# Performance work log

Hardware: AMD Instinct MI355X
Metric: run time of the kernel (lower is better)

The kernel has to match this reference:

```python
import jax, jax.numpy as jnp
import numpy as np

N_LAYERS = 12
N_HEADS = 12
D_MODEL = 768
VOCAB = 50257
T_WIN = 1024
B, T = 4, 1024
STD = 0.02


def setup_inputs() -> dict:
    key = jax.random.key(0)
    ks = jax.random.split(key, 8)
    inp = jax.random.randint(ks[0], (B, T), 0, VOCAB)
    target = jax.random.randint(ks[1], (B, T), 0, VOCAB)
    wte = jax.random.normal(ks[2], (VOCAB, D_MODEL), jnp.float32) * STD
    wpe = jax.random.normal(ks[3], (T_WIN, D_MODEL), jnp.float32) * STD
    attn_w = jax.random.normal(ks[4], (N_LAYERS, D_MODEL, 3 * D_MODEL), jnp.float32) * STD
    proj_w = jax.random.normal(ks[5], (N_LAYERS, D_MODEL, D_MODEL), jnp.float32) * STD
    fc_w = jax.random.normal(ks[6], (N_LAYERS, D_MODEL, 4 * D_MODEL), jnp.float32) * STD
    fc2_w = jax.random.normal(ks[7], (N_LAYERS, 4 * D_MODEL, D_MODEL), jnp.float32) * STD
    return {
        'inp': inp, 'target': target, 'wte': wte, 'wpe': wpe,
        'ln1_w': jnp.ones((N_LAYERS, D_MODEL), jnp.float32),
        'ln1_b': jnp.zeros((N_LAYERS, D_MODEL), jnp.float32),
        'attn_w': attn_w,
        'attn_b': jnp.zeros((N_LAYERS, 3 * D_MODEL), jnp.float32),
        'proj_w': proj_w,
        'proj_b': jnp.zeros((N_LAYERS, D_MODEL), jnp.float32),
        'ln2_w': jnp.ones((N_LAYERS, D_MODEL), jnp.float32),
        'ln2_b': jnp.zeros((N_LAYERS, D_MODEL), jnp.float32),
        'fc_w': fc_w,
        'fc_b': jnp.zeros((N_LAYERS, 4 * D_MODEL), jnp.float32),
        'fc2_w': fc2_w,
        'fc2_b': jnp.zeros((N_LAYERS, D_MODEL), jnp.float32),
        'lnf_w': jnp.ones((D_MODEL,), jnp.float32),
        'lnf_b': jnp.zeros((D_MODEL,), jnp.float32),
    }


def _layernorm(x, w, b, eps=1e-5):
    mu = jnp.mean(x, axis=-1, keepdims=True)
    var = jnp.var(x, axis=-1, keepdims=True)
    return (x - mu) * jax.lax.rsqrt(var + eps) * w + b


def _attention(x, w_qkv, b_qkv, w_proj, b_proj):
    b, t, c = x.shape
    hd = c // N_HEADS
    qkv = x @ w_qkv + b_qkv                      # [B,T,3C]
    q, k, v = jnp.split(qkv, 3, axis=-1)
    # [B,H,T,hd]
    q = q.reshape(b, t, N_HEADS, hd).transpose(0, 2, 1, 3)
    k = k.reshape(b, t, N_HEADS, hd).transpose(0, 2, 1, 3)
    v = v.reshape(b, t, N_HEADS, hd).transpose(0, 2, 1, 3)
    scores = jnp.einsum('bhqd,bhkd->bhqk', q, k) / jnp.sqrt(jnp.float32(hd))
    causal = jnp.tril(jnp.ones((t, t), bool))
    scores = jnp.where(causal[None, None], scores, -jnp.inf)
    w = jax.nn.softmax(scores, axis=-1)          # dropout p=0 (eval)
    ctx = jnp.einsum('bhqk,bhkd->bhqd', w, v)
    ctx = ctx.transpose(0, 2, 1, 3).reshape(b, t, c)
    return ctx @ w_proj + b_proj


def reference(inp, target, wte, wpe, ln1_w, ln1_b, attn_w, attn_b, proj_w, proj_b,
              ln2_w, ln2_b, fc_w, fc_b, fc2_w, fc2_b, lnf_w, lnf_b):
    b, t = inp.shape
    x = wte[inp] + wpe[:t][None]                 # [B,T,C]
    for i in range(N_LAYERS):
        x = x + _attention(_layernorm(x, ln1_w[i], ln1_b[i]),
                           attn_w[i], attn_b[i], proj_w[i], proj_b[i])
        h = _layernorm(x, ln2_w[i], ln2_b[i])
        h = jax.nn.gelu(h @ fc_w[i] + fc_b[i], approximate=True)
        x = x + (h @ fc2_w[i] + fc2_b[i])
    x = _layernorm(x, lnf_w, lnf_b)
    logits = x @ wte.T                            # tied lm_head, no bias
    logp = jax.nn.log_softmax(logits, axis=-1)
    nll = -jnp.take_along_axis(logp, target[..., None], axis=-1)[..., 0]
    loss = jnp.mean(nll)
    return logits, loss
```

## Files before the change

kernel.cpp:

```cpp
#include <hip/hip_runtime.h>
#include <hip/hip_bf16.h>
#include <cmath>

#define NLAYERS 12
#define NHEADS  12
#define DM      768
#define VOCAB   50257
#define TSEQ    1024
#define BT      4096
#define NCHUNK  786

typedef __attribute__((ext_vector_type(4))) float f32x4;
typedef __attribute__((ext_vector_type(8))) short bf16x8;

typedef __hip_bfloat16 bf16;

#define MFMA16(a, b, c) __builtin_amdgcn_mfma_f32_16x16x32_bf16(a, b, c, 0, 0, 0)

__device__ __forceinline__ void gload16(const void* g, void* l) {
    __builtin_amdgcn_global_load_lds(
        (const __attribute__((address_space(1))) void*)g,
        (__attribute__((address_space(3))) void*)l, 16, 0, 0);
}

__device__ __forceinline__ void wg_barrier() {
    asm volatile("" ::: "memory");
    __builtin_amdgcn_s_barrier();
    asm volatile("" ::: "memory");
}

__device__ __forceinline__ float gelu_tanh(float v) {
    float u = 0.7978845608028654f * (v + 0.044715f * v * v * v);
    return 0.5f * v * (1.0f + tanhf(u));
}

__device__ __forceinline__ short f2bf(float f) {
    bf16 h = (bf16)f;
    return *reinterpret_cast<short*>(&h);
}

struct ushort4s { short a, b, c, d; };

__global__ void transpose_bf16_kernel(const float* __restrict__ in, bf16* __restrict__ out,
                                      int K, int N) {
    __shared__ float tile[32][33];
    size_t lofs = (size_t)blockIdx.z * K * N;
    int k0 = blockIdx.y * 32, n0 = blockIdx.x * 32;
    int tx = threadIdx.x, ty = threadIdx.y;
#pragma unroll
    for (int i = 0; i < 32; i += 8)
        tile[ty + i][tx] = in[lofs + (size_t)(k0 + ty + i) * N + n0 + tx];
    __syncthreads();
#pragma unroll
    for (int i = 0; i < 32; i += 8)
        out[lofs + (size_t)(n0 + ty + i) * K + k0 + tx] = (bf16)tile[tx][ty + i];
}

__global__ void tobf16_kernel(const float* __restrict__ in, bf16* __restrict__ out, size_t n) {
    size_t i = (size_t)blockIdx.x * 256 + threadIdx.x;
    if (i < n) out[i] = (bf16)in[i];
}

__global__ void embed_kernel(const int* __restrict__ inp, const float* __restrict__ wte,
                             const float* __restrict__ wpe, float* __restrict__ x) {
    int idx = blockIdx.x * 256 + threadIdx.x;
    int m = idx / (DM / 4), c4 = idx % (DM / 4);
    int tok = inp[m];
    int t = m & (TSEQ - 1);
    float4 a = reinterpret_cast<const float4*>(wte)[(size_t)tok * (DM / 4) + c4];
    float4 b = reinterpret_cast<const float4*>(wpe)[(size_t)t * (DM / 4) + c4];
    float4 o = {a.x + b.x, a.y + b.y, a.z + b.z, a.w + b.w};
    reinterpret_cast<float4*>(x)[idx] = o;
}

__global__ __launch_bounds__(256) void ln_kernel(const float* __restrict__ x,
                                                 const float* __restrict__ w,
                                                 const float* __restrict__ b,
                                                 bf16* __restrict__ y) {
    int row = blockIdx.x, tid = threadIdx.x;
    const float4* xr = reinterpret_cast<const float4*>(x + (size_t)row * DM);
    float4 v = {0.f, 0.f, 0.f, 0.f};
    float s = 0.f, q = 0.f;
    if (tid < 192) {
        v = xr[tid];
        s = v.x + v.y + v.z + v.w;
        q = v.x * v.x + v.y * v.y + v.z * v.z + v.w * v.w;
    }
#pragma unroll
    for (int o = 1; o < 64; o <<= 1) { s += __shfl_xor(s, o); q += __shfl_xor(q, o); }
    __shared__ float ss[4], qq[4];
    if ((tid & 63) == 0) { ss[tid >> 6] = s; qq[tid >> 6] = q; }
    __syncthreads();
    s = ss[0] + ss[1] + ss[2] + ss[3];
    q = qq[0] + qq[1] + qq[2] + qq[3];
    float mu  = s * (1.0f / DM);
    float var = q * (1.0f / DM) - mu * mu;
    float inv = rsqrtf(var + 1e-5f);
    if (tid < 192) {
        float4 wv = reinterpret_cast<const float4*>(w)[tid];
        float4 bv = reinterpret_cast<const float4*>(b)[tid];
        ushort4s o;
        o.a = f2bf((v.x - mu) * inv * wv.x + bv.x);
        o.b = f2bf((v.y - mu) * inv * wv.y + bv.y);
        o.c = f2bf((v.z - mu) * inv * wv.z + bv.z);
        o.d = f2bf((v.w - mu) * inv * wv.w + bv.w);
        *reinterpret_cast<ushort4s*>(y + (size_t)row * DM + tid * 4) = o;
    }
}

#define GF_GELU    1
#define GF_OBF16   2
#define GF_CLAMP   4
#define GF_PARTIAL 8

template<int FLAGS, int TAG>
__global__ __launch_bounds__(256) void gemm_k(
    const bf16* __restrict__ A, const bf16* __restrict__ Bt,
    const float* __restrict__ bias, const float* __restrict__ resid,
    void* __restrict__ C, float2* __restrict__ partials,
    int M, int N, int K) {
    __shared__ short ldsA[2][128 * 32];
    __shared__ short ldsB[2][128 * 32];
    int tid = threadIdx.x;
    int lane = tid & 63, w = tid >> 6;
    int wm = w >> 1, wn = w & 1;
    int r = lane & 15, kq = lane >> 4;
    int bm = blockIdx.x * 128, bn = blockIdx.y * 128;

    f32x4 acc[4][4] = {};

    auto stage = [&](int buf, int k0) {
#pragma unroll
        for (int i = 0; i < 2; ++i) {
            int chunk = i * 256 + tid;
            int row = chunk >> 2;
            int gs = (chunk & 3) ^ ((row >> 1) & 3);
            const bf16* ga = A + (size_t)(bm + row) * K + k0 + gs * 8;
            gload16(ga, &ldsA[buf][(i * 256 + w * 64) * 8]);
            int brow = bn + row;
            if (FLAGS & GF_CLAMP) brow = min(brow, N - 1);
            const bf16* gb = Bt + (size_t)brow * K + k0 + gs * 8;
            gload16(gb, &ldsB[buf][(i * 256 + w * 64) * 8]);
        }
    };
    auto compute = [&](int buf) {
        bf16x8 af[4], bfr[4];
#pragma unroll
        for (int m = 0; m < 4; ++m) {
            int row = wm * 64 + m * 16 + r;
            af[m] = *reinterpret_cast<bf16x8*>(&ldsA[buf][row * 32 + (kq ^ ((row >> 1) & 3)) * 8]);
        }
#pragma unroll
        for (int n = 0; n < 4; ++n) {
            int row = wn * 64 + n * 16 + r;
            bfr[n] = *reinterpret_cast<bf16x8*>(&ldsB[buf][row * 32 + (kq ^ ((row >> 1) & 3)) * 8]);
        }
#pragma unroll
        for (int m = 0; m < 4; ++m)
#pragma unroll
            for (int n = 0; n < 4; ++n)
                acc[m][n] = MFMA16(af[m], bfr[n], acc[m][n]);
    };

    stage(0, 0);
    __syncthreads();
    int buf = 0;
    for (int k0 = 32; k0 < K; k0 += 32) {
        stage(buf ^ 1, k0);
        compute(buf);
        __syncthreads();
        buf ^= 1;
    }
    compute(buf);

    int row0 = bm + wm * 64, col0 = bn + wn * 64;
#pragma unroll
    for (int m = 0; m < 4; ++m) {
#pragma unroll
        for (int n = 0; n < 4; ++n) {
            int col = col0 + n * 16 + r;
            if (col < N) {
#pragma unroll
                for (int rr = 0; rr < 4; ++rr) {
                    int row = row0 + m * 16 + kq * 4 + rr;
                    float v = acc[m][n][rr];
                    if (bias) v += bias[col];
                    if (FLAGS & GF_GELU) v = gelu_tanh(v);
                    if (resid) v += resid[(size_t)row * N + col];
                    if (FLAGS & GF_OBF16) ((bf16*)C)[(size_t)row * N + col] = (bf16)v;
                    else                  ((float*)C)[(size_t)row * N + col] = v;
                }
            }
        }
    }
}

template<int FLAGS, int TAG>
__global__ __launch_bounds__(512, 1) void gemm256_8p(
    const bf16* __restrict__ A, const bf16* __restrict__ Bt,
    const float* __restrict__ bias, const float* __restrict__ resid,
    void* __restrict__ C, float2* __restrict__ partials,
    int M, int N, int K) {
    __shared__ short lds[2][2][256 * 64];
    int tid = threadIdx.x;
    int lane = tid & 63, w = tid >> 6;
    int wm = w >> 2, wn = w & 3;
    int r = lane & 15, kq = lane >> 4;
    int bm = blockIdx.x * 256, bn = blockIdx.y * 256;

    f32x4 acc[8][4] = {};

    auto stage_half = [&](int buf, int kt, int half) {
        int mat = half >> 1;
        int hrow = (half & 1) * 128;
        const bf16* src = mat ? Bt : A;
        int base = mat ? bn : bm;
#pragma unroll
        for (int i = 0; i < 2; ++i) {
            int chunk = i * 512 + tid;
            int lrow = hrow + (chunk >> 3);
            int gsrc = (chunk & 7) ^ (lrow & 7);
            int grow = base + lrow;
            if (mat && (FLAGS & GF_CLAMP)) grow = min(grow, N - 1);
            gload16(src + (size_t)grow * K + kt * 64 + gsrc * 8,
                    &lds[buf][mat][hrow * 64 + chunk * 8]);
        }
    };

    auto do_phase = [&](int buf, int p) {
        int mh = p >> 1, nh = p & 1;
        bf16x8 bfr[2][2], af[4][2];
#pragma unroll
        for (int n2 = 0; n2 < 2; ++n2) {
            int row = wn * 64 + (nh * 2 + n2) * 16 + r;
#pragma unroll
            for (int kk = 0; kk < 2; ++kk) {
                int lg = kk * 4 + kq;
                bfr[n2][kk] = *reinterpret_cast<bf16x8*>(
                    &lds[buf][1][row * 64 + (lg ^ (row & 7)) * 8]);
            }
        }
#pragma unroll
        for (int m2 = 0; m2 < 4; ++m2) {
            int row = wm * 128 + (mh * 4 + m2) * 16 + r;
#pragma unroll
            for (int kk = 0; kk < 2; ++kk) {
                int lg = kk * 4 + kq;
                af[m2][kk] = *reinterpret_cast<bf16x8*>(
                    &lds[buf][0][row * 64 + (lg ^ (row & 7)) * 8]);
            }
        }
        __builtin_amdgcn_s_setprio(1);
#pragma unroll
        for (int m2 = 0; m2 < 4; ++m2)
#pragma unroll
            for (int n2 = 0; n2 < 2; ++n2)
#pragma unroll
                for (int kk = 0; kk < 2; ++kk)
                    acc[mh * 4 + m2][nh * 2 + n2] =
                        MFMA16(af[m2][kk], bfr[n2][kk], acc[mh * 4 + m2][nh * 2 + n2]);
        __builtin_amdgcn_s_setprio(0);
    };

    const int NT = K / 64;
    stage_half(0, 0, 0); stage_half(0, 0, 1); stage_half(0, 0, 2); stage_half(0, 0, 3);
    for (int t = 0; t < NT; ++t) {
        int buf = t & 1;
        bool more = (t + 1 < NT);
        if (more) { stage_half(buf ^ 1, t + 1, 0); stage_half(buf ^ 1, t + 1, 1); }
        if (more) asm volatile("s_waitcnt vmcnt(4)" ::: "memory");
        else      asm volatile("s_waitcnt vmcnt(0)" ::: "memory");
        wg_barrier();
        do_phase(buf, 0);
        wg_barrier();
        if (more) { stage_half(buf ^ 1, t + 1, 2); stage_half(buf ^ 1, t + 1, 3); }
        do_phase(buf, 1);
        wg_barrier();
        do_phase(buf, 2);
        wg_barrier();
        do_phase(buf, 3);
        wg_barrier();
    }

    int row0 = bm + wm * 128, col0 = bn + wn * 64;
#pragma unroll
    for (int m = 0; m < 8; ++m) {
#pragma unroll
        for (int n = 0; n < 4; ++n) {
            int col = col0 + n * 16 + r;
            if (col < N) {
#pragma unroll
                for (int rr = 0; rr < 4; ++rr) {
                    int row = row0 + m * 16 + kq * 4 + rr;
                    float v = acc[m][n][rr];
                    if (bias) v += bias[col];
                    if (FLAGS & GF_GELU) v = gelu_tanh(v);
                    if (resid) v += resid[(size_t)row * N + col];
                    if (FLAGS & GF_OBF16) ((bf16*)C)[(size_t)row * N + col] = (bf16)v;
                    else                  ((float*)C)[(size_t)row * N + col] = v;
                }
            }
        }
    }

    if (FLAGS & GF_PARTIAL) {
        int chunk = (bn >> 6) + wn;
        if (chunk < NCHUNK) {
#pragma unroll
            for (int m = 0; m < 8; ++m) {
#pragma unroll
                for (int rr = 0; rr < 4; ++rr) {
                    float vals[4], mx = -INFINITY;
#pragma unroll
                    for (int n = 0; n < 4; ++n) {
                        int col = col0 + n * 16 + r;
                        float v = (col < N) ? acc[m][n][rr] : -INFINITY;
                        vals[n] = v;
                        mx = fmaxf(mx, v);
                    }
#pragma unroll
                    for (int o = 1; o < 16; o <<= 1) mx = fmaxf(mx, __shfl_xor(mx, o));
                    float sum = 0.f;
#pragma unroll
                    for (int n = 0; n < 4; ++n)
                        if (vals[n] > -INFINITY) sum += __expf(vals[n] - mx);
#pragma unroll
                    for (int o = 1; o < 16; o <<= 1) sum += __shfl_xor(sum, o);
                    if (r == 0) {
                        int row = row0 + m * 16 + kq * 4 + rr;
                        partials[(size_t)row * NCHUNK + chunk] = make_float2(mx, sum);
                    }
                }
            }
        }
    }
}

__global__ __launch_bounds__(256) void flash_attn_kernel(const bf16* __restrict__ qkv,
                                                         bf16* __restrict__ ctx) {
    __shared__ short Ks[128 * 64];
    __shared__ short Vt[64][132];
    __shared__ short Ps[4][16][132];

    int tid = threadIdx.x, lane = tid & 63, w = tid >> 6;
    int r = lane & 15, kq = lane >> 4;
    int q0 = blockIdx.x * 64;
    int bh = blockIdx.y;
    int b = bh / NHEADS, h = bh % NHEADS;
    const int RS = 3 * DM;

    const bf16* qbase = qkv + (size_t)(b * TSEQ + q0 + w * 16 + r) * RS + h * 64;
    bf16x8 qf[2];
    qf[0] = *reinterpret_cast<const bf16x8*>(qbase + kq * 8);
    qf[1] = *reinterpret_cast<const bf16x8*>(qbase + 32 + kq * 8);

    f32x4 of[4] = {};
    float mrow[4] = {-INFINITY, -INFINITY, -INFINITY, -INFINITY};
    float lrow[4] = {};

    int ntiles = (blockIdx.x >> 1) + 1;
    for (int t = 0; t < ntiles; ++t) {
        int kv0 = t * 128;
        __syncthreads();
        const bf16* kbase = qkv + (size_t)(b * TSEQ + kv0) * RS + DM + h * 64;
#pragma unroll
        for (int i = 0; i < 4; ++i) {
            int chunk = i * 256 + tid;
            int row = chunk >> 3, cp = chunk & 7;
            int csrc = cp ^ (row & 7);
            gload16(kbase + (size_t)row * RS + csrc * 8, Ks + chunk * 8);
        }
        const bf16* vbase = qkv + (size_t)(b * TSEQ + kv0) * RS + 2 * DM + h * 64;
#pragma unroll
        for (int i = 0; i < 4; ++i) {
            int chunk = i * 256 + tid;
            int kv = chunk >> 3, d0 = (chunk & 7) * 8;
            bf16x8 v = *reinterpret_cast<const bf16x8*>(vbase + (size_t)kv * RS + d0);
#pragma unroll
            for (int j = 0; j < 8; ++j) Vt[d0 + j][kv] = ((short*)&v)[j];
        }
        __syncthreads();

        f32x4 sf[8];
#pragma unroll
        for (int n = 0; n < 8; ++n) sf[n] = (f32x4){0.f, 0.f, 0.f, 0.f};
        __builtin_amdgcn_s_setprio(1);
#pragma unroll
        for (int n = 0; n < 8; ++n) {
            int row = n * 16 + r;
#pragma unroll
            for (int kt = 0; kt < 2; ++kt) {
                int gran = (kt * 4 + kq) ^ (row & 7);
                bf16x8 kf = *reinterpret_cast<bf16x8*>(&Ks[row * 64 + gran * 8]);
                sf[n] = MFMA16(qf[kt], kf, sf[n]);
            }
        }
        __builtin_amdgcn_s_setprio(0);

        bool diag = (kv0 + 128 > q0);
        float alpha[4];
#pragma unroll
        for (int rr = 0; rr < 4; ++rr) {
            int qrow = q0 + w * 16 + kq * 4 + rr;
            float vals[8];
            float mx = mrow[rr];
#pragma unroll
            for (int n = 0; n < 8; ++n) {
                float v = sf[n][rr] * 0.125f;
                if (diag && (kv0 + n * 16 + r) > qrow) v = -INFINITY;
                vals[n] = v;
                mx = fmaxf(mx, v);
            }
#pragma unroll
            for (int o = 1; o < 16; o <<= 1) mx = fmaxf(mx, __shfl_xor(mx, o));
            float al = __expf(mrow[rr] - mx);
            float sum = 0.f;
#pragma unroll
            for (int n = 0; n < 8; ++n) {
                float p = __expf(vals[n] - mx);
                vals[n] = p;
                sum += p;
            }
#pragma unroll
            for (int o = 1; o < 16; o <<= 1) sum += __shfl_xor(sum, o);
            mrow[rr] = mx;
            lrow[rr] = lrow[rr] * al + sum;
            alpha[rr] = al;
#pragma unroll
            for (int n = 0; n < 8; ++n) Ps[w][kq * 4 + rr][n * 16 + r] = f2bf(vals[n]);
        }
#pragma unroll
        for (int n = 0; n < 4; ++n)
#pragma unroll
            for (int rr = 0; rr < 4; ++rr) of[n][rr] *= alpha[rr];

        __builtin_amdgcn_s_setprio(1);
#pragma unroll
        for (int kt = 0; kt < 4; ++kt) {
            bf16x8 pa = *reinterpret_cast<bf16x8*>(&Ps[w][r][kt * 32 + kq * 8]);
#pragma unroll
            for (int n = 0; n < 4; ++n) {
                bf16x8 vf = *reinterpret_cast<bf16x8*>(&Vt[n * 16 + r][kt * 32 + kq * 8]);
                of[n] = MFMA16(pa, vf, of[n]);
            }
        }
        __builtin_amdgcn_s_setprio(0);
    }

#pragma unroll
    for (int rr = 0; rr < 4; ++rr) {
        float inv = 1.0f / lrow[rr];
        int qrow = q0 + w * 16 + kq * 4 + rr;
        bf16* cb = ctx + (size_t)(b * TSEQ + qrow) * DM + h * 64;
#pragma unroll
        for (int n = 0; n < 4; ++n) cb[n * 16 + r] = (bf16)(of[n][rr] * inv);
    }
}

__global__ __launch_bounds__(256) void loss_reduce_kernel(const float2* __restrict__ partials,
                                                          const float* __restrict__ logits,
                                                          const int* __restrict__ target,
                                                          float* __restrict__ nll) {
    int row = blockIdx.x, tid = threadIdx.x;
    const float2* pr = partials + (size_t)row * NCHUNK;
    float m = -INFINITY, s = 0.f;
    for (int c = tid; c < NCHUNK; c += 256) {
        float2 p = pr[c];
        if (p.x > m) { s = s * __expf(m - p.x) + p.y; m = p.x; }
        else         { s += p.y * __expf(p.x - m); }
    }
    __shared__ float sm[256], ssum[256];
    sm[tid] = m; ssum[tid] = s; __syncthreads();
    for (int o = 128; o; o >>= 1) {
        if (tid < o) {
            float m2 = sm[tid + o], s2 = ssum[tid + o];
            float mm = fmaxf(sm[tid], m2);
            ssum[tid] = ssum[tid] * __expf(sm[tid] - mm) + s2 * __expf(m2 - mm);
            sm[tid] = mm;
        }
        __syncthreads();
    }
    if (tid == 0) {
        float lse = sm[0] + logf(ssum[0]);
        nll[row] = lse - logits[(size_t)row * VOCAB + target[row]];
    }
}

__global__ void loss2_kernel(const float* __restrict__ nll, float* __restrict__ loss) {
    int tid = threadIdx.x;
    float s = 0.f;
    for (int i = tid; i < BT; i += 1024) s += nll[i];
    __shared__ float r[1024];
    r[tid] = s; __syncthreads();
    for (int o = 512; o; o >>= 1) { if (tid < o) r[tid] += r[tid + o]; __syncthreads(); }
    if (tid == 0) *loss = r[0] * (1.0f / BT);
}

extern "C" void kernel_launch(void* const* d_in, const int* in_sizes, int n_in,
                              void* d_out, int out_size, void* d_ws, size_t ws_size,
                              hipStream_t stream) {
    const int*   inp    = (const int*)  d_in[0];
    const int*   target = (const int*)  d_in[1];
    const float* wte    = (const float*)d_in[2];
    const float* wpe    = (const float*)d_in[3];
    const float* ln1_w  = (const float*)d_in[4];
    const float* ln1_b  = (const float*)d_in[5];
    const float* attn_w = (const float*)d_in[6];
    const float* attn_b = (const float*)d_in[7];
    const float* proj_w = (const float*)d_in[8];
    const float* proj_b = (const float*)d_in[9];
    const float* ln2_w  = (const float*)d_in[10];
    const float* ln2_b  = (const float*)d_in[11];
    const float* fc_w   = (const float*)d_in[12];
    const float* fc_b   = (const float*)d_in[13];
    const float* fc2_w  = (const float*)d_in[14];
    const float* fc2_b  = (const float*)d_in[15];
    const float* lnf_w  = (const float*)d_in[16];
    const float* lnf_b  = (const float*)d_in[17];
    float* out = (float*)d_out;

    char* p = (char*)d_ws;
    auto alloc = [&](size_t bytes) { char* q = p; p += (bytes + 255) & ~(size_t)255; return q; };
    float* x     = (float*)alloc((size_t)BT * DM * 4);
    float* nll   = (float*)alloc((size_t)BT * 4);
    bf16*  qkvb  = (bf16*) alloc((size_t)BT * 3 * DM * 2);
    bf16*  tmpb  = (bf16*) alloc((size_t)BT * DM * 2);
    bf16*  ctxb  = (bf16*) alloc((size_t)BT * DM * 2);
    bf16*  hb    = (bf16*) alloc((size_t)BT * 4 * DM * 2);
    bf16*  wteb  = (bf16*) alloc((size_t)VOCAB * DM * 2);
    bf16*  wqkvT = (bf16*) alloc((size_t)NLAYERS * 3 * DM * DM * 2);
    bf16*  wprojT= (bf16*) alloc((size_t)NLAYERS * DM * DM * 2);
    bf16*  wfcT  = (bf16*) alloc((size_t)NLAYERS * 4 * DM * DM * 2);
    bf16*  wfc2T = (bf16*) alloc((size_t)NLAYERS * 4 * DM * DM * 2);
    float2* partials = (float2*)ctxb;

    dim3 tb(32, 8);
    transpose_bf16_kernel<<<dim3(3 * DM / 32, DM / 32, NLAYERS), tb, 0, stream>>>(attn_w, wqkvT, DM, 3 * DM);
    transpose_bf16_kernel<<<dim3(DM / 32, DM / 32, NLAYERS), tb, 0, stream>>>(proj_w, wprojT, DM, DM);
    transpose_bf16_kernel<<<dim3(4 * DM / 32, DM / 32, NLAYERS), tb, 0, stream>>>(fc_w, wfcT, DM, 4 * DM);
    transpose_bf16_kernel<<<dim3(DM / 32, 4 * DM / 32, NLAYERS), tb, 0, stream>>>(fc2_w, wfc2T, 4 * DM, DM);
    {
        size_t n = (size_t)VOCAB * DM;
        tobf16_kernel<<<(unsigned)((n + 255) / 256), 256, 0, stream>>>(wte, wteb, n);
    }

    embed_kernel<<<BT * DM / 4 / 256, 256, 0, stream>>>(inp, wte, wpe, x);

    for (int i = 0; i < NLAYERS; ++i) {
        ln_kernel<<<BT, 256, 0, stream>>>(x, ln1_w + i * DM, ln1_b + i * DM, tmpb);
        gemm_k<GF_OBF16, 0><<<dim3(BT / 128, 3 * DM / 128), 256, 0, stream>>>(
            tmpb, wqkvT + (size_t)i * 3 * DM * DM, attn_b + i * 3 * DM, nullptr,
            qkvb, nullptr, BT, 3 * DM, DM);
        flash_attn_kernel<<<dim3(TSEQ / 64, 4 * NHEADS), 256, 0, stream>>>(qkvb, ctxb);
        gemm_k<0, 1><<<dim3(BT / 128, DM / 128), 256, 0, stream>>>(
            ctxb, wprojT + (size_t)i * DM * DM, proj_b + i * DM, x,
            x, nullptr, BT, DM, DM);
        ln_kernel<<<BT, 256, 0, stream>>>(x, ln2_w + i * DM, ln2_b + i * DM, tmpb);
        gemm_k<GF_GELU | GF_OBF16, 2><<<dim3(BT / 128, 4 * DM / 128), 256, 0, stream>>>(
            tmpb, wfcT + (size_t)i * 4 * DM * DM, fc_b + i * 4 * DM, nullptr,
            hb, nullptr, BT, 4 * DM, DM);
        gemm_k<0, 3><<<dim3(BT / 128, DM / 128), 256, 0, stream>>>(
            hb, wfc2T + (size_t)i * 4 * DM * DM, fc2_b + i * DM, x,
            x, nullptr, BT, DM, 4 * DM);
    }

    ln_kernel<<<BT, 256, 0, stream>>>(x, lnf_w, lnf_b, tmpb);
    gemm256_8p<GF_CLAMP | GF_PARTIAL, 4><<<dim3(BT / 256, (VOCAB + 255) / 256), 512, 0, stream>>>(
        tmpb, wteb, nullptr, nullptr, out, partials, BT, VOCAB, DM);
    loss_reduce_kernel<<<BT, 256, 0, stream>>>(partials, out, target, nll);
    loss2_kernel<<<1, 1024, 0, stream>>>(nll, out + (size_t)out_size - 1);
}
```

Baseline: 4.290 ms.

## Software-pipeline GEMM fragment loads and swizzle V transpose in flash attention

The 256x256 GEMM now loads the LDS fragments for the next phase while the current phase's MFMAs run, and prefetches the next tile's first fragments at the end of each iteration. The global-load wait moves later in the loop, and launch bounds are raised to allow two blocks per CU. Flash attention now builds the transposed V tile with 4-element packed stores into an XOR-swizzled layout instead of scalar stores into a padded array, to cut LDS bank conflicts and store count. The cost is higher register pressure from holding two fragment sets, which may conflict with the 2-block occupancy target and cause spills.

```diff
diff --git a/kernel.cpp b/kernel.cpp
--- a/kernel.cpp
+++ b/kernel.cpp
@@ -12,6 +12,7 @@
 
 typedef __attribute__((ext_vector_type(4))) float f32x4;
 typedef __attribute__((ext_vector_type(8))) short bf16x8;
+typedef __attribute__((ext_vector_type(4))) short s16x4;
 
 typedef __hip_bfloat16 bf16;
 
@@ -196,7 +197,7 @@
 }
 
 template<int FLAGS, int TAG>
-__global__ __launch_bounds__(512, 1) void gemm256_8p(
+__global__ __launch_bounds__(512, 2) void gemm256_8p(
     const bf16* __restrict__ A, const bf16* __restrict__ Bt,
     const float* __restrict__ bias, const float* __restrict__ resid,
     void* __restrict__ C, float2* __restrict__ partials,
@@ -227,29 +228,30 @@
         }
     };
 
-    auto do_phase = [&](int buf, int p) {
+    struct Frags { bf16x8 a[4][2]; bf16x8 b[2][2]; };
+
+    auto ld_frags = [&](int buf, int p, Frags& F) {
         int mh = p >> 1, nh = p & 1;
-        bf16x8 bfr[2][2], af[4][2];
 #pragma unroll
         for (int n2 = 0; n2 < 2; ++n2) {
             int row = wn * 64 + (nh * 2 + n2) * 16 + r;
 #pragma unroll
-            for (int kk = 0; kk < 2; ++kk) {
-                int lg = kk * 4 + kq;
-                bfr[n2][kk] = *reinterpret_cast<bf16x8*>(
-                    &lds[buf][1][row * 64 + (lg ^ (row & 7)) * 8]);
-            }
+            for (int kk = 0; kk < 2; ++kk)
+                F.b[n2][kk] = *reinterpret_cast<bf16x8*>(
+                    &lds[buf][1][row * 64 + ((kk * 4 + kq) ^ (row & 7)) * 8]);
         }
 #pragma unroll
         for (int m2 = 0; m2 < 4; ++m2) {
             int row = wm * 128 + (mh * 4 + m2) * 16 + r;
 #pragma unroll
-            for (int kk = 0; kk < 2; ++kk) {
-                int lg = kk * 4 + kq;
-                af[m2][kk] = *reinterpret_cast<bf16x8*>(
-                    &lds[buf][0][row * 64 + (lg ^ (row & 7)) * 8]);
-            }
-        }
+            for (int kk = 0; kk < 2; ++kk)
+                F.a[m2][kk] = *reinterpret_cast<bf16x8*>(
+                    &lds[buf][0][row * 64 + ((kk * 4 + kq) ^ (row & 7)) * 8]);
+        }
+    };
+
+    auto do_mfma = [&](int p, Frags& F) {
+        int mh = p >> 1, nh = p & 1;
         __builtin_amdgcn_s_setprio(1);
 #pragma unroll
         for (int m2 = 0; m2 < 4; ++m2)
@@ -258,27 +260,34 @@
 #pragma unroll
                 for (int kk = 0; kk < 2; ++kk)
                     acc[mh * 4 + m2][nh * 2 + n2] =
-                        MFMA16(af[m2][kk], bfr[n2][kk], acc[mh * 4 + m2][nh * 2 + n2]);
+                        MFMA16(F.a[m2][kk], F.b[n2][kk], acc[mh * 4 + m2][nh * 2 + n2]);
         __builtin_amdgcn_s_setprio(0);
     };
 
     const int NT = K / 64;
     stage_half(0, 0, 0); stage_half(0, 0, 1); stage_half(0, 0, 2); stage_half(0, 0, 3);
+    asm volatile("s_waitcnt vmcnt(0)" ::: "memory");
+    wg_barrier();
+    Frags cur, nxt;
+    ld_frags(0, 0, cur);
+
     for (int t = 0; t < NT; ++t) {
         int buf = t & 1;
         bool more = (t + 1 < NT);
+        do_mfma(0, cur);
         if (more) { stage_half(buf ^ 1, t + 1, 0); stage_half(buf ^ 1, t + 1, 1); }
-        if (more) asm volatile("s_waitcnt vmcnt(4)" ::: "memory");
-        else      asm volatile("s_waitcnt vmcnt(0)" ::: "memory");
+        ld_frags(buf, 1, nxt);
         wg_barrier();
-        do_phase(buf, 0);
+        do_mfma(1, nxt);
+        if (more) { stage_half(buf ^ 1, t + 1, 2); stage_half(buf ^ 1, t + 1, 3); }
+        ld_frags(buf, 2, cur);
         wg_barrier();
-        if (more) { stage_half(buf ^ 1, t + 1, 2); stage_half(buf ^ 1, t + 1, 3); }
-        do_phase(buf, 1);
+        do_mfma(2, cur);
+        if (more) asm volatile("s_waitcnt vmcnt(0)" ::: "memory");
+        ld_frags(buf, 3, nxt);
         wg_barrier();
-        do_phase(buf, 2);
-        wg_barrier();
-        do_phase(buf, 3);
+        do_mfma(3, nxt);
+        if (more) ld_frags(buf ^ 1, 0, cur);
         wg_barrier();
     }
 
@@ -339,7 +348,7 @@
 __global__ __launch_bounds__(256) void flash_attn_kernel(const bf16* __restrict__ qkv,
                                                          bf16* __restrict__ ctx) {
     __shared__ short Ks[128 * 64];
-    __shared__ short Vt[64][132];
+    __shared__ short Vt[64 * 128];
     __shared__ short Ps[4][16][132];
 
     int tid = threadIdx.x, lane = tid & 63, w = tid >> 6;
@@ -371,13 +380,21 @@
             gload16(kbase + (size_t)row * RS + csrc * 8, Ks + chunk * 8);
         }
         const bf16* vbase = qkv + (size_t)(b * TSEQ + kv0) * RS + 2 * DM + h * 64;
-#pragma unroll
-        for (int i = 0; i < 4; ++i) {
-            int chunk = i * 256 + tid;
-            int kv = chunk >> 3, d0 = (chunk & 7) * 8;
-            bf16x8 v = *reinterpret_cast<const bf16x8*>(vbase + (size_t)kv * RS + d0);
-#pragma unroll
-            for (int j = 0; j < 8; ++j) Vt[d0 + j][kv] = ((short*)&v)[j];
+        {
+            int kvq = tid >> 3;
+            int d0 = (tid & 7) * 8;
+            bf16x8 v0 = *reinterpret_cast<const bf16x8*>(vbase + (size_t)(kvq * 4 + 0) * RS + d0);
+            bf16x8 v1 = *reinterpret_cast<const bf16x8*>(vbase + (size_t)(kvq * 4 + 1) * RS + d0);
+            bf16x8 v2 = *reinterpret_cast<const bf16x8*>(vbase + (size_t)(kvq * 4 + 2) * RS + d0);
+            bf16x8 v3 = *reinterpret_cast<const bf16x8*>(vbase + (size_t)(kvq * 4 + 3) * RS + d0);
+            int lg = kvq >> 1, half = kvq & 1;
+#pragma unroll
+            for (int j = 0; j < 8; ++j) {
+                int d = d0 + j;
+                int phys = lg ^ (d & 7);
+                s16x4 pk = {v0[j], v1[j], v2[j], v3[j]};
+                *reinterpret_cast<s16x4*>(&Vt[d * 128 + phys * 8 + half * 4]) = pk;
+            }
         }
         __syncthreads();
 
@@ -440,7 +457,9 @@
             bf16x8 pa = *reinterpret_cast<bf16x8*>(&Ps[w][r][kt * 32 + kq * 8]);
 #pragma unroll
             for (int n = 0; n < 4; ++n) {
-                bf16x8 vf = *reinterpret_cast<bf16x8*>(&Vt[n * 16 + r][kt * 32 + kq * 8]);
+                int row = n * 16 + r;
+                int gran = (kt * 4 + kq) ^ (row & 7);
+                bf16x8 vf = *reinterpret_cast<bf16x8*>(&Vt[row * 128 + gran * 8]);
                 of[n] = MFMA16(pa, vf, of[n]);
             }
         }
```

After: 4.341 ms. About the same (+1.2%).

## Prefetch K/V via registers in flash attention and use one-wave-per-row layernorm

Applied to the files above, without the earlier changes.

Flash attention now loads the next K/V tile into registers while the current tile computes, then writes K and a transposed V into LDS using a swizzled layout without padding. The goal is to hide global load latency and cut bank conflicts on the V transpose. LayerNorm now processes four rows per block, one wavefront per row, which removes the LDS reduction and the block barrier. The register prefetch raises VGPR pressure in the attention kernel and could lower occupancy.

```diff
diff --git a/kernel.cpp b/kernel.cpp
--- a/kernel.cpp
+++ b/kernel.cpp
@@ -12,6 +12,7 @@
 
 typedef __attribute__((ext_vector_type(4))) float f32x4;
 typedef __attribute__((ext_vector_type(8))) short bf16x8;
+typedef __attribute__((ext_vector_type(4))) short s16x4;
 
 typedef __hip_bfloat16 bf16;
 
@@ -77,34 +78,33 @@
                                                  const float* __restrict__ w,
                                                  const float* __restrict__ b,
                                                  bf16* __restrict__ y) {
-    int row = blockIdx.x, tid = threadIdx.x;
+    int tid = threadIdx.x, wv = tid >> 6, lane = tid & 63;
+    int row = blockIdx.x * 4 + wv;
     const float4* xr = reinterpret_cast<const float4*>(x + (size_t)row * DM);
-    float4 v = {0.f, 0.f, 0.f, 0.f};
+    float4 v[3];
     float s = 0.f, q = 0.f;
-    if (tid < 192) {
-        v = xr[tid];
-        s = v.x + v.y + v.z + v.w;
-        q = v.x * v.x + v.y * v.y + v.z * v.z + v.w * v.w;
+#pragma unroll
+    for (int j = 0; j < 3; ++j) {
+        v[j] = xr[lane + 64 * j];
+        s += v[j].x + v[j].y + v[j].z + v[j].w;
+        q += v[j].x * v[j].x + v[j].y * v[j].y + v[j].z * v[j].z + v[j].w * v[j].w;
     }
 #pragma unroll
     for (int o = 1; o < 64; o <<= 1) { s += __shfl_xor(s, o); q += __shfl_xor(q, o); }
-    __shared__ float ss[4], qq[4];
-    if ((tid & 63) == 0) { ss[tid >> 6] = s; qq[tid >> 6] = q; }
-    __syncthreads();
-    s = ss[0] + ss[1] + ss[2] + ss[3];
-    q = qq[0] + qq[1] + qq[2] + qq[3];
     float mu  = s * (1.0f / DM);
     float var = q * (1.0f / DM) - mu * mu;
     float inv = rsqrtf(var + 1e-5f);
-    if (tid < 192) {
-        float4 wv = reinterpret_cast<const float4*>(w)[tid];
-        float4 bv = reinterpret_cast<const float4*>(b)[tid];
+#pragma unroll
+    for (int j = 0; j < 3; ++j) {
+        int c4 = lane + 64 * j;
+        float4 wv4 = reinterpret_cast<const float4*>(w)[c4];
+        float4 bv4 = reinterpret_cast<const float4*>(b)[c4];
         ushort4s o;
-        o.a = f2bf((v.x - mu) * inv * wv.x + bv.x);
-        o.b = f2bf((v.y - mu) * inv * wv.y + bv.y);
-        o.c = f2bf((v.z - mu) * inv * wv.z + bv.z);
-        o.d = f2bf((v.w - mu) * inv * wv.w + bv.w);
-        *reinterpret_cast<ushort4s*>(y + (size_t)row * DM + tid * 4) = o;
+        o.a = f2bf((v[j].x - mu) * inv * wv4.x + bv4.x);
+        o.b = f2bf((v[j].y - mu) * inv * wv4.y + bv4.y);
+        o.c = f2bf((v[j].z - mu) * inv * wv4.z + bv4.z);
+        o.d = f2bf((v[j].w - mu) * inv * wv4.w + bv4.w);
+        *reinterpret_cast<ushort4s*>(y + (size_t)row * DM + c4 * 4) = o;
     }
 }
 
@@ -234,21 +234,17 @@
         for (int n2 = 0; n2 < 2; ++n2) {
             int row = wn * 64 + (nh * 2 + n2) * 16 + r;
 #pragma unroll
-            for (int kk = 0; kk < 2; ++kk) {
-                int lg = kk * 4 + kq;
+            for (int kk = 0; kk < 2; ++kk)
                 bfr[n2][kk] = *reinterpret_cast<bf16x8*>(
-                    &lds[buf][1][row * 64 + (lg ^ (row & 7)) * 8]);
-            }
+                    &lds[buf][1][row * 64 + ((kk * 4 + kq) ^ (row & 7)) * 8]);
         }
 #pragma unroll
         for (int m2 = 0; m2 < 4; ++m2) {
             int row = wm * 128 + (mh * 4 + m2) * 16 + r;
 #pragma unroll
-            for (int kk = 0; kk < 2; ++kk) {
-                int lg = kk * 4 + kq;
+            for (int kk = 0; kk < 2; ++kk)
                 af[m2][kk] = *reinterpret_cast<bf16x8*>(
-                    &lds[buf][0][row * 64 + (lg ^ (row & 7)) * 8]);
-            }
+                    &lds[buf][0][row * 64 + ((kk * 4 + kq) ^ (row & 7)) * 8]);
         }
         __builtin_amdgcn_s_setprio(1);
 #pragma unroll
@@ -339,7 +335,7 @@
 __global__ __launch_bounds__(256) void flash_attn_kernel(const bf16* __restrict__ qkv,
                                                          bf16* __restrict__ ctx) {
     __shared__ short Ks[128 * 64];
-    __shared__ short Vt[64][132];
+    __shared__ short Vt[64 * 128];
     __shared__ short Ps[4][16][132];
 
     int tid = threadIdx.x, lane = tid & 63, w = tid >> 6;
@@ -358,29 +354,51 @@
     float mrow[4] = {-INFINITY, -INFINITY, -INFINITY, -INFINITY};
     float lrow[4] = {};
 
+    int kvq = tid >> 3;
+    int d0 = (tid & 7) * 8;
+    const bf16* kbase0 = qkv + (size_t)(b * TSEQ) * RS + DM + h * 64;
+    const bf16* vbase0 = qkv + (size_t)(b * TSEQ) * RS + 2 * DM + h * 64;
+    bf16x8 kr0, kr1, kr2, kr3, vr0, vr1, vr2, vr3;
+
+    auto loadKV = [&](int t) {
+        const bf16* kb = kbase0 + (size_t)(t * 128 + kvq * 4) * RS + d0;
+        const bf16* vb = vbase0 + (size_t)(t * 128 + kvq * 4) * RS + d0;
+        kr0 = *reinterpret_cast<const bf16x8*>(kb);
+        kr1 = *reinterpret_cast<const bf16x8*>(kb + RS);
+        kr2 = *reinterpret_cast<const bf16x8*>(kb + 2 * RS);
+        kr3 = *reinterpret_cast<const bf16x8*>(kb + 3 * RS);
+        vr0 = *reinterpret_cast<const bf16x8*>(vb);
+        vr1 = *reinterpret_cast<const bf16x8*>(vb + RS);
+        vr2 = *reinterpret_cast<const bf16x8*>(vb + 2 * RS);
+        vr3 = *reinterpret_cast<const bf16x8*>(vb + 3 * RS);
+    };
+    auto writeKV = [&]() {
+        bf16x8 krs[4] = {kr0, kr1, kr2, kr3};
+#pragma unroll
+        for (int j = 0; j < 4; ++j) {
+            int kv = kvq * 4 + j;
+            int pg = (tid & 7) ^ (kv & 7);
+            *reinterpret_cast<bf16x8*>(&Ks[kv * 64 + pg * 8]) = krs[j];
+        }
+        int lg = kvq >> 1, half = kvq & 1;
+#pragma unroll
+        for (int jj = 0; jj < 8; ++jj) {
+            int d = d0 + jj;
+            int phys = lg ^ (d & 7);
+            s16x4 pk = {vr0[jj], vr1[jj], vr2[jj], vr3[jj]};
+            *reinterpret_cast<s16x4*>(&Vt[d * 128 + phys * 8 + half * 4]) = pk;
+        }
+    };
+
     int ntiles = (blockIdx.x >> 1) + 1;
+    loadKV(0);
     for (int t = 0; t < ntiles; ++t) {
+        __syncthreads();
+        writeKV();
+        __syncthreads();
+        if (t + 1 < ntiles) loadKV(t + 1);
+
         int kv0 = t * 128;
-        __syncthreads();
-        const bf16* kbase = qkv + (size_t)(b * TSEQ + kv0) * RS + DM + h * 64;
-#pragma unroll
-        for (int i = 0; i < 4; ++i) {
-            int chunk = i * 256 + tid;
-            int row = chunk >> 3, cp = chunk & 7;
-            int csrc = cp ^ (row & 7);
-            gload16(kbase + (size_t)row * RS + csrc * 8, Ks + chunk * 8);
-        }
-        const bf16* vbase = qkv + (size_t)(b * TSEQ + kv0) * RS + 2 * DM + h * 64;
-#pragma unroll
-        for (int i = 0; i < 4; ++i) {
-            int chunk = i * 256 + tid;
-            int kv = chunk >> 3, d0 = (chunk & 7) * 8;
-            bf16x8 v = *reinterpret_cast<const bf16x8*>(vbase + (size_t)kv * RS + d0);
-#pragma unroll
-            for (int j = 0; j < 8; ++j) Vt[d0 + j][kv] = ((short*)&v)[j];
-        }
-        __syncthreads();
-
         f32x4 sf[8];
 #pragma unroll
         for (int n = 0; n < 8; ++n) sf[n] = (f32x4){0.f, 0.f, 0.f, 0.f};
@@ -440,7 +458,9 @@
             bf16x8 pa = *reinterpret_cast<bf16x8*>(&Ps[w][r][kt * 32 + kq * 8]);
 #pragma unroll
             for (int n = 0; n < 4; ++n) {
-                bf16x8 vf = *reinterpret_cast<bf16x8*>(&Vt[n * 16 + r][kt * 32 + kq * 8]);
+                int row = n * 16 + r;
+                int gran = (kt * 4 + kq) ^ (row & 7);
+                bf16x8 vf = *reinterpret_cast<bf16x8*>(&Vt[row * 128 + gran * 8]);
                 of[n] = MFMA16(pa, vf, of[n]);
             }
         }
@@ -547,7 +567,7 @@
     embed_kernel<<<BT * DM / 4 / 256, 256, 0, stream>>>(inp, wte, wpe, x);
 
     for (int i = 0; i < NLAYERS; ++i) {
-        ln_kernel<<<BT, 256, 0, stream>>>(x, ln1_w + i * DM, ln1_b + i * DM, tmpb);
+        ln_kernel<<<BT / 4, 256, 0, stream>>>(x, ln1_w + i * DM, ln1_b + i * DM, tmpb);
         gemm_k<GF_OBF16, 0><<<dim3(BT / 128, 3 * DM / 128), 256, 0, stream>>>(
             tmpb, wqkvT + (size_t)i * 3 * DM * DM, attn_b + i * 3 * DM, nullptr,
             qkvb, nullptr, BT, 3 * DM, DM);
@@ -555,7 +575,7 @@
         gemm_k<0, 1><<<dim3(BT / 128, DM / 128), 256, 0, stream>>>(
             ctxb, wprojT + (size_t)i * DM * DM, proj_b + i * DM, x,
             x, nullptr, BT, DM, DM);
-        ln_kernel<<<BT, 256, 0, stream>>>(x, ln2_w + i * DM, ln2_b + i * DM, tmpb);
+        ln_kernel<<<BT / 4, 256, 0, stream>>>(x, ln2_w + i * DM, ln2_b + i * DM, tmpb);
         gemm_k<GF_GELU | GF_OBF16, 2><<<dim3(BT / 128, 4 * DM / 128), 256, 0, stream>>>(
             tmpb, wfcT + (size_t)i * 4 * DM * DM, fc_b + i * 4 * DM, nullptr,
             hb, nullptr, BT, 4 * DM, DM);
@@ -564,7 +584,7 @@
             x, nullptr, BT, DM, 4 * DM);
     }
 
-    ln_kernel<<<BT, 256, 0, stream>>>(x, lnf_w, lnf_b, tmpb);
+    ln_kernel<<<BT / 4, 256, 0, stream>>>(x, lnf_w, lnf_b, tmpb);
     gemm256_8p<GF_CLAMP | GF_PARTIAL, 4><<<dim3(BT / 256, (VOCAB + 255) / 256), 512, 0, stream>>>(
         tmpb, wteb, nullptr, nullptr, out, partials, BT, VOCAB, DM);
     loss_reduce_kernel<<<BT, 256, 0, stream>>>(partials, out, target, nll);
```

New measurement: 4.262 ms. No clear change (-0.7%).
